# Optimization experiments

Hardware: AMD Instinct MI355X
Metric: run time of the kernel (lower is better)

Reference implementation:

```python
import jax, jax.numpy as jnp
import numpy as np

NUM_HEADS = 8
TEMPERATURE = 10000.0


def sine_embed(pos, dim):
    """Sine positional embedding of 2D offsets. pos [..., 2] -> [..., dim]."""
    half = dim // 2  # dims per coordinate
    dim_t = TEMPERATURE ** (2.0 * (jnp.arange(half) // 2).astype(jnp.float32) / half)
    s = pos[..., :, None] / dim_t  # [..., 2, half]
    emb = jnp.stack([jnp.sin(s[..., 0::2]), jnp.cos(s[..., 1::2])], axis=-1)
    emb = emb.reshape(s.shape[:-1] + (half,))  # interleaved sin/cos per coord
    return emb.reshape(pos.shape[:-1] + (dim,))


def setup_inputs() -> dict:
    key = jax.random.key(0)
    ks = jax.random.split(key, 16)
    N, H, W, C, K = 2, 40, 40, 256, 100
    h = NUM_HEADS
    sc = 1.0 / np.sqrt(C)
    return {
        "query_feature": jax.random.normal(ks[0], (N, H, W, C), jnp.float32),
        "query_position": jax.random.uniform(ks[1], (N, H, W, 2), jnp.float32),
        "key_feature": jax.random.normal(ks[2], (N, K, C), jnp.float32),
        "key_position": jax.random.uniform(ks[3], (N, K, 2), jnp.float32),
        # MultiheadAttention params (torch convention: weight [out, in])
        "in_proj_w": jax.random.normal(ks[4], (3 * C, C), jnp.float32) * sc,
        "in_proj_b": jnp.zeros((3 * C,), jnp.float32),
        "out_proj_w": jax.random.normal(ks[5], (C, C), jnp.float32) * sc,
        "out_proj_b": jnp.zeros((C,), jnp.float32),
        # PositionalEncodingSineLearned MLP: sine(C) -> C -> num_heads
        "pos_w1": jax.random.normal(ks[6], (C, C), jnp.float32) * sc,
        "pos_b1": jnp.zeros((C,), jnp.float32),
        "pos_w2": jax.random.normal(ks[7], (h, C), jnp.float32) * sc,
        "pos_b2": jnp.zeros((h,), jnp.float32),
        # cat_pos branch params
        "pos_trans_w": jax.random.normal(ks[8], (2, 2), jnp.float32),
        "embed_w": jax.random.normal(ks[9], (C, C + 2), jnp.float32) * 0.01,
        "embed_b": jnp.zeros((C,), jnp.float32),
    }


def reference(query_feature, query_position, key_feature, key_position,
              in_proj_w, in_proj_b, out_proj_w, out_proj_b,
              pos_w1, pos_b1, pos_w2, pos_b2,
              pos_trans_w, embed_w, embed_b):
    N, H, W, C = query_feature.shape
    h = NUM_HEADS
    d = C // h
    q = query_feature.reshape(N, -1, C)            # [N,Q,C]
    qp = query_position.reshape(N, -1, 2)          # [N,Q,2] (scale_terms = 1.0)
    Q = q.shape[1]
    K = key_feature.shape[1]

    # pairwise relative positions: [N,Q,K,2]
    rel_pos = key_position[:, None, :, :] - qp[:, :, None, :]

    # learned sine relative positional encoding -> per-head additive bias
    pe = sine_embed(rel_pos, C)                              # [N,Q,K,C]
    hid = jax.nn.relu(pe @ pos_w1.T + pos_b1)                # [N,Q,K,C]
    bias = (hid @ pos_w2.T + pos_b2).transpose(0, 3, 1, 2)   # [N,h,Q,K]

    # multihead attention with additive relative bias
    wq, wk, wv = jnp.split(in_proj_w, 3, axis=0)
    bq, bk, bv = jnp.split(in_proj_b, 3, axis=0)
    qh = ((q @ wq.T + bq).reshape(N, Q, h, d)) * (d ** -0.5)
    kh = (key_feature @ wk.T + bk).reshape(N, K, h, d)
    vh = (key_feature @ wv.T + bv).reshape(N, K, h, d)
    scores = jnp.einsum('nqhd,nkhd->nhqk', qh, kh) + bias
    attn = jax.nn.softmax(scores, axis=-1)                   # [N,h,Q,K]
    ctx = jnp.einsum('nhqk,nkhd->nqhd', attn, vh).reshape(N, Q, C)
    refined = ctx @ out_proj_w.T + out_proj_b                # [N,Q,C]

    # cat_pos: attention-weighted relative position aggregation
    attn_w = attn.mean(axis=1)                               # [N,Q,K]
    new_rel = jnp.einsum('nqk,nqkc->nqc', attn_w, jax.lax.stop_gradient(rel_pos))
    new_pos = new_rel @ pos_trans_w.T                        # [N,Q,2]

    feat = jax.nn.relu(q + refined)
    feat = jax.nn.relu(jnp.concatenate([feat, new_pos], axis=-1) @ embed_w.T + embed_b)
    return feat.reshape(N, H, W, C)
```

## Files before the change

### kernel.cpp

```cpp
#include <hip/hip_runtime.h>
#include <math.h>

typedef __bf16 bf16x8 __attribute__((ext_vector_type(8)));
typedef __bf16 bf16x4 __attribute__((ext_vector_type(4)));
typedef float  f32x4  __attribute__((ext_vector_type(4)));


#define WS_KH    0u
#define WS_VH    51200u
#define WS_EWP   102400u
#define WS_QHB   168960u
#define WS_BIASB 578560u
#define WS_KEB   2012160u
#define WS_W1B   2038560u
#define WS_W2PB  2071328u

__device__ __forceinline__ float rdlane(float v, int l) {
  return __uint_as_float(__builtin_amdgcn_readlane(__float_as_uint(v), l));
}

__global__ __launch_bounds__(256, 2) void prep_kernel(
    const float* __restrict__ qfeat, const float* __restrict__ kfeat,
    const float* __restrict__ kpos,
    const float* __restrict__ ipw, const float* __restrict__ ipb,
    const float* __restrict__ pos_w1, const float* __restrict__ pos_w2,
    const float* __restrict__ embed_w, float* __restrict__ ws)
{
  __shared__ float x[8 * 256];
  int bid = blockIdx.x, t = threadIdx.x;

  if (bid < 50) {
    int r = bid * 4 + (t >> 6);
    int u = t & 63;
    float p0 = kpos[r * 2 + 0], p1 = kpos[r * 2 + 1];
    __bf16* keb = (__bf16*)(ws + WS_KEB);
    bf16x4 o;
#pragma unroll
    for (int j = 0; j < 4; j++) {
      int col = u * 4 + j;
      int c = col >> 7, i = (col & 127) >> 1;
      float p = c ? p1 : p0;
      float inv = exp2f((float)i * (-13.287712379549449f / 64.0f));
      float v = p * inv;
      o[j] = (__bf16)((col & 1) ? __cosf(v) : __sinf(v));
    }
    *(bf16x4*)(keb + r * 264 + u * 4) = o;
  } else if (bid < 114) {
    int idx = (bid - 50) * 1024 + t * 4;
    float4 v = *(const float4*)(pos_w1 + idx);
    bf16x4 o; o[0] = (__bf16)v.x; o[1] = (__bf16)v.y; o[2] = (__bf16)v.z; o[3] = (__bf16)v.w;
    *(bf16x4*)((__bf16*)(ws + WS_W1B) + idx) = o;
  } else if (bid == 114) {
    __bf16* w2pb = (__bf16*)(ws + WS_W2PB);
    for (int i = 0; i < 16; i++) {
      int idx = t * 16 + i;
      w2pb[idx] = (idx < 2048) ? (__bf16)pos_w2[idx] : (__bf16)0.0f;
    }
  } else if (bid < 147) {
    int r0 = (bid - 115) * 8;
    for (int rr = 0; rr < 8; rr++) {
      int r = r0 + rr;
      for (int j = t; j < 260; j += 256)
        ws[WS_EWP + r * 260 + j] = (j < 258) ? embed_w[r * 258 + j] : 0.0f;
    }
  } else if (bid < 547) {
    int r0 = (bid - 147) * 8;
    for (int i = t; i < 2048; i += 256) x[i] = qfeat[(unsigned)r0 * 256u + i];
    __syncthreads();
    float acc[8]; float bq = ipb[t];
#pragma unroll
    for (int rr = 0; rr < 8; rr++) acc[rr] = bq;
    const float* wrow = ipw + (unsigned)t * 256u;
    for (int j = 0; j < 256; j += 4) {
      float4 w4 = *(const float4*)(wrow + j);
#pragma unroll
      for (int rr = 0; rr < 8; rr++) {
        float4 x4 = *(const float4*)(x + rr * 256 + j);
        acc[rr] = fmaf(x4.x, w4.x, fmaf(x4.y, w4.y, fmaf(x4.z, w4.z, fmaf(x4.w, w4.w, acc[rr]))));
      }
    }
    __bf16* qhb = (__bf16*)(ws + WS_QHB);
#pragma unroll
    for (int rr = 0; rr < 8; rr++)
      qhb[(unsigned)(r0 + rr) * 256u + t] = (__bf16)(acc[rr] * 0.17677669529663687f);
  } else {
    int b2 = bid - 547; int n = b2 >> 4, tile = b2 & 15;
    int r0l = tile * 7; int cnt = 100 - r0l; if (cnt > 7) cnt = 7; if (cnt <= 0) return;
    int r0 = n * 100 + r0l;
    for (int i = t; i < cnt * 256; i += 256) x[i] = kfeat[(unsigned)r0 * 256u + i];
    __syncthreads();
    float ak[7], av[7]; float bk = ipb[256 + t], bv = ipb[512 + t];
#pragma unroll
    for (int rr = 0; rr < 7; rr++) { ak[rr] = bk; av[rr] = bv; }
    const float* wkr = ipw + (unsigned)(256 + t) * 256u;
    const float* wvr = ipw + (unsigned)(512 + t) * 256u;
    for (int j = 0; j < 256; j += 4) {
      float4 wk4 = *(const float4*)(wkr + j);
      float4 wv4 = *(const float4*)(wvr + j);
#pragma unroll
      for (int rr = 0; rr < 7; rr++) {
        float4 x4 = *(const float4*)(x + rr * 256 + j);
        ak[rr] = fmaf(x4.x, wk4.x, fmaf(x4.y, wk4.y, fmaf(x4.z, wk4.z, fmaf(x4.w, wk4.w, ak[rr]))));
        av[rr] = fmaf(x4.x, wv4.x, fmaf(x4.y, wv4.y, fmaf(x4.z, wv4.z, fmaf(x4.w, wv4.w, av[rr]))));
      }
    }
    for (int rr = 0; rr < 7; rr++) {
      if (rr < cnt) {
        ws[WS_KH + (unsigned)(r0 + rr) * 256u + t] = ak[rr];
        ws[WS_VH + (unsigned)(r0 + rr) * 256u + t] = av[rr];
      }
    }
  }
}

__global__ __launch_bounds__(512) void bias_kernel(
    const float* __restrict__ qpos,
    const float* __restrict__ pos_b1, const float* __restrict__ pos_b2,
    float* __restrict__ ws)
{
  __shared__ __align__(16) char smem[63488];
  __bf16* qe_s   = (__bf16*)(smem + 28672);
  __bf16* region = (__bf16*)(smem + 30720);

  int bid = blockIdx.x;
  int n = bid / 400;
  int q0 = bid * 4;
  int t = threadIdx.x;
  int lane = t & 63, w = t >> 6;
  int l15 = lane & 15, quad = lane >> 4;

  const __bf16* keb = (const __bf16*)(ws + WS_KEB) + (unsigned)(n * 100) * 264u;
  const __bf16* w1b = (const __bf16*)(ws + WS_W1B);
  const __bf16* w2pb = (const __bf16*)(ws + WS_W2PB);
  __bf16* biasb = (__bf16*)(ws + WS_BIASB);

  {
    int idx = t * 2;
    int q = idx >> 8, u = idx & 255;
    int c = u >> 7, i = (u & 127) >> 1;
    float p = qpos[(q0 + q) * 2 + c];
    float inv = exp2f((float)i * (-13.287712379549449f / 64.0f));
    float v = p * inv;
    qe_s[idx]     = (__bf16)__sinf(v);
    qe_s[idx + 1] = (__bf16)__cosf(v);
  }

  bf16x8 wfrag[2][8];
#pragma unroll
  for (int ct = 0; ct < 2; ct++)
#pragma unroll
    for (int kc = 0; kc < 8; kc++)
      wfrag[ct][kc] = *(const bf16x8*)(w1b + (unsigned)(w * 32 + ct * 16 + l15) * 256u + kc * 32 + quad * 8);
  float b1v[2][4];
#pragma unroll
  for (int ct = 0; ct < 2; ct++)
#pragma unroll
    for (int r = 0; r < 4; r++) b1v[ct][r] = pos_b1[w * 32 + ct * 16 + quad * 4 + r];
  float b2v[4];
#pragma unroll
  for (int r = 0; r < 4; r++) b2v[r] = pos_b2[(quad * 4 + r) & 7];

  auto gen = [&](int q, int pair, int buf) {
    if (t < 448) {
      int key = t >> 2, sub = t & 3;
      int cb = pair * 64 + sub * 16;
      bf16x8 fr0, fr1;
      const __bf16* qp = qe_s + q * 256 + cb;
      bf16x8 q0f = *(const bf16x8*)qp;
      bf16x8 q1f = *(const bf16x8*)(qp + 8);
      if (key < 100) {
        const __bf16* kp = keb + (unsigned)key * 264u + cb;
        bf16x8 k0f = *(const bf16x8*)kp;
        bf16x8 k1f = *(const bf16x8*)(kp + 8);
#pragma unroll
        for (int jj = 0; jj < 4; jj++) {
          float sk = (float)k0f[2 * jj], ck = (float)k0f[2 * jj + 1];
          float sq = (float)q0f[2 * jj], cq = (float)q0f[2 * jj + 1];
          fr0[2 * jj]     = (__bf16)(sk * cq - ck * sq);
          fr0[2 * jj + 1] = (__bf16)(ck * cq + sk * sq);
          float sk1 = (float)k1f[2 * jj], ck1 = (float)k1f[2 * jj + 1];
          float sq1 = (float)q1f[2 * jj], cq1 = (float)q1f[2 * jj + 1];
          fr1[2 * jj]     = (__bf16)(sk1 * cq1 - ck1 * sq1);
          fr1[2 * jj + 1] = (__bf16)(ck1 * cq1 + sk1 * sq1);
        }
      } else {
#pragma unroll
        for (int jj = 0; jj < 8; jj++) { fr0[jj] = (__bf16)0.f; fr1[jj] = (__bf16)0.f; }
      }
      int mt = key >> 4, kl = key & 15;
      int kcl = sub >> 1;
      int qd0 = (sub & 1) * 2;
      bf16x8* base = (bf16x8*)smem + buf * 896 + kcl * 448 + mt * 64;
      base[qd0 * 16 + (kl ^ (qd0 * 2 + kcl))]             = fr0;
      base[(qd0 + 1) * 16 + (kl ^ (qd0 * 2 + 2 + kcl))]   = fr1;
    }
  };

  f32x4 zero4; zero4[0] = 0.f; zero4[1] = 0.f; zero4[2] = 0.f; zero4[3] = 0.f;

  __syncthreads();
  gen(0, 0, 0);
  __syncthreads();

  for (int q = 0; q < 4; q++) {
    f32x4 acc[2][7];
#pragma unroll
    for (int ct = 0; ct < 2; ct++)
#pragma unroll
      for (int mt = 0; mt < 7; mt++) acc[ct][mt] = zero4;

    for (int p = 0; p < 4; p++) {
      if (p < 3) gen(q, p + 1, (p + 1) & 1);
      else if (q < 3) gen(q + 1, 0, 0);
      const bf16x8* pb = (const bf16x8*)smem + (p & 1) * 896;
#pragma unroll
      for (int kh = 0; kh < 2; kh++) {
        int kc = p * 2 + kh;
        bf16x8 pf[7];
#pragma unroll
        for (int mt = 0; mt < 7; mt++)
          pf[mt] = pb[kh * 448 + mt * 64 + quad * 16 + (l15 ^ (quad * 2 + kh))];
#pragma unroll
        for (int mt = 0; mt < 7; mt++) {
          acc[0][mt] = __builtin_amdgcn_mfma_f32_16x16x32_bf16(wfrag[0][kc], pf[mt], acc[0][mt], 0, 0, 0);
          acc[1][mt] = __builtin_amdgcn_mfma_f32_16x16x32_bf16(wfrag[1][kc], pf[mt], acc[1][mt], 0, 0, 0);
        }
      }
      __syncthreads();
    }

#pragma unroll
    for (int ct = 0; ct < 2; ct++)
#pragma unroll
      for (int mt = 0; mt < 7; mt++)
#pragma unroll
        for (int r = 0; r < 4; r++)
          acc[ct][mt][r] = fmaxf(acc[ct][mt][r] + b1v[ct][r], 0.0f);

    auto wreg = [&](int mt, int slot) {
#pragma unroll
      for (int ct = 0; ct < 2; ct++) {
        int qt = ct * 2 + (quad >> 1);
        int j0 = (quad & 1) * 4;
        bf16x4 o;
#pragma unroll
        for (int r = 0; r < 4; r++) o[r] = (__bf16)acc[ct][mt][r];
        *(bf16x4*)(region + slot * 4096 + ((w * 64 + qt * 16 + l15) << 3) + j0) = o;
      }
    };
    auto g2 = [&](int mt, int slot) {
      f32x4 acc2 = zero4;
      const bf16x8* rg = (const bf16x8*)(region + slot * 4096);
#pragma unroll
      for (int s = 0; s < 8; s++) {
        bf16x8 w2f = *(const bf16x8*)(w2pb + (unsigned)l15 * 256u + s * 32 + quad * 8);
        bf16x8 hf = rg[s * 64 + lane];
        acc2 = __builtin_amdgcn_mfma_f32_16x16x32_bf16(w2f, hf, acc2, 0, 0, 0);
      }
      if (quad < 2) {
        bf16x4 o;
#pragma unroll
        for (int r = 0; r < 4; r++) o[r] = (__bf16)(acc2[r] + b2v[r]);
        *(bf16x4*)(biasb + ((unsigned)(q0 + q) * 112u + mt * 16 + l15) * 8u + quad * 4) = o;
      }
    };

    wreg(0, 0); wreg(1, 1); wreg(2, 2); wreg(3, 3);
    __syncthreads();
    if (w < 4) g2(w, w);
    __syncthreads();
    wreg(4, 0); wreg(5, 1); wreg(6, 2);
    __syncthreads();
    if (w < 3) g2(4 + w, w);
  }
}

__global__ __launch_bounds__(256, 4) void attn_kernel(
    const float* __restrict__ qfeat, const float* __restrict__ qpos,
    const float* __restrict__ kpos,
    const float* __restrict__ out_w, const float* __restrict__ out_b,
    const float* __restrict__ embed_b, const float* __restrict__ ptw,
    const float* __restrict__ ws, float* __restrict__ out)
{
  __shared__ float qh_s[4 * 8 * 36];
  __shared__ float attn_s[4 * 8 * 116];
  __shared__ float ctx_s[4 * 264];
  __shared__ float cat_s[4 * 264];
  __shared__ float aw_s[4 * 104];

  int bid = blockIdx.x;
  int qg0 = bid * 4;
  int n = bid / 400;
  int t = threadIdx.x;

  const __bf16* qhb = (const __bf16*)(ws + WS_QHB);
  const __bf16* biasb = (const __bf16*)(ws + WS_BIASB);
  const float* kh = ws + WS_KH;
  const float* vh = ws + WS_VH;
  const float* ewp = ws + WS_EWP;

  for (int i = t; i < 1024; i += 256) {
    int q = i >> 8, c = i & 255;
    qh_s[(q * 8 + (c >> 5)) * 36 + (c & 31)] = (float)qhb[(unsigned)(qg0 + q) * 256u + c];
  }
  __syncthreads();

  for (int i = 0; i < 4; i++) {
    int p = t + i * 256;
    if (p < 800) {
      int k = p >> 3, h = p & 7;
      const float4* kf = (const float4*)(kh + (unsigned)(n * 100 + k) * 256u + h * 32);
      float4 kv[8];
#pragma unroll
      for (int dd = 0; dd < 8; dd++) kv[dd] = kf[dd];
#pragma unroll
      for (int q = 0; q < 4; q++) {
        const float4* qf = (const float4*)(qh_s + (q * 8 + h) * 36);
        float s = (float)biasb[((unsigned)(qg0 + q) * 112u + k) * 8u + h];
#pragma unroll
        for (int dd = 0; dd < 8; dd++) {
          float4 qv = qf[dd];
          s += kv[dd].x * qv.x + kv[dd].y * qv.y + kv[dd].z * qv.z + kv[dd].w * qv.w;
        }
        attn_s[(q * 8 + h) * 116 + k] = s;
      }
    }
  }
  __syncthreads();

  {
    int q = t >> 6, h = (t >> 3) & 7, j = t & 7;
    float* row = attn_s + (q * 8 + h) * 116;
    float mx = -1e30f;
    for (int k = j; k < 100; k += 8) mx = fmaxf(mx, row[k]);
    mx = fmaxf(mx, __shfl_xor(mx, 1, 8));
    mx = fmaxf(mx, __shfl_xor(mx, 2, 8));
    mx = fmaxf(mx, __shfl_xor(mx, 4, 8));
    float sum = 0.f;
    for (int k = j; k < 100; k += 8) { float e = __expf(row[k] - mx); row[k] = e; sum += e; }
    sum += __shfl_xor(sum, 1, 8);
    sum += __shfl_xor(sum, 2, 8);
    sum += __shfl_xor(sum, 4, 8);
    float inv = 1.0f / sum;
    for (int k = j; k < 100; k += 8) row[k] *= inv;
  }
  __syncthreads();

  for (int p = t; p < 416; p += 256) {
    int q = p / 104, k = p % 104;
    if (k < 100) {
      float s = 0.f;
#pragma unroll
      for (int h = 0; h < 8; h++) s += attn_s[(q * 8 + h) * 116 + k];
      aw_s[q * 104 + k] = s * 0.125f;
    }
  }
  {
    int c = t, h = c >> 5;
    float a0 = 0.f, a1 = 0.f, a2 = 0.f, a3 = 0.f;
    const float* vp = vh + (unsigned)(n * 100) * 256u + c;
    const float* r0 = attn_s + (0 * 8 + h) * 116;
    const float* r1 = attn_s + (1 * 8 + h) * 116;
    const float* r2 = attn_s + (2 * 8 + h) * 116;
    const float* r3 = attn_s + (3 * 8 + h) * 116;
#pragma unroll 4
    for (int k = 0; k < 100; k++) {
      float vv = vp[(unsigned)k * 256u];
      a0 = fmaf(r0[k], vv, a0);
      a1 = fmaf(r1[k], vv, a1);
      a2 = fmaf(r2[k], vv, a2);
      a3 = fmaf(r3[k], vv, a3);
    }
    ctx_s[0 * 264 + c] = a0; ctx_s[1 * 264 + c] = a1;
    ctx_s[2 * 264 + c] = a2; ctx_s[3 * 264 + c] = a3;
  }
  __syncthreads();

  if (t < 8) {
    int q = t >> 1, cd = t & 1;
    float qp = qpos[(qg0 + q) * 2 + cd];
    float s = 0.f;
    for (int k = 0; k < 100; k++)
      s = fmaf(aw_s[q * 104 + k], kpos[(n * 100 + k) * 2 + cd] - qp, s);
    float so = __shfl_xor(s, 1, 2);
    if (cd == 0) cat_s[q * 264 + 256] = ptw[0] * s + ptw[1] * so;
    else         cat_s[q * 264 + 257] = ptw[2] * so + ptw[3] * s;
  }

  {
    int c = t, lane = t & 63;
    float ob = out_b[c];
    float acc0 = ob, acc1 = ob, acc2 = ob, acc3 = ob;
    const float* wr = out_w + (unsigned)c * 256u;
    for (int ch = 0; ch < 4; ch++) {
      float v0 = ctx_s[0 * 264 + ch * 64 + lane];
      float v1 = ctx_s[1 * 264 + ch * 64 + lane];
      float v2 = ctx_s[2 * 264 + ch * 64 + lane];
      float v3 = ctx_s[3 * 264 + ch * 64 + lane];
      const float* wp = wr + ch * 64;
#pragma unroll 4
      for (int j4 = 0; j4 < 16; j4++) {
        float4 w4 = *(const float4*)(wp + j4 * 4);
        int jb = j4 * 4;
        acc0 = fmaf(rdlane(v0, jb + 0), w4.x, acc0);
        acc1 = fmaf(rdlane(v1, jb + 0), w4.x, acc1);
        acc2 = fmaf(rdlane(v2, jb + 0), w4.x, acc2);
        acc3 = fmaf(rdlane(v3, jb + 0), w4.x, acc3);
        acc0 = fmaf(rdlane(v0, jb + 1), w4.y, acc0);
        acc1 = fmaf(rdlane(v1, jb + 1), w4.y, acc1);
        acc2 = fmaf(rdlane(v2, jb + 1), w4.y, acc2);
        acc3 = fmaf(rdlane(v3, jb + 1), w4.y, acc3);
        acc0 = fmaf(rdlane(v0, jb + 2), w4.z, acc0);
        acc1 = fmaf(rdlane(v1, jb + 2), w4.z, acc1);
        acc2 = fmaf(rdlane(v2, jb + 2), w4.z, acc2);
        acc3 = fmaf(rdlane(v3, jb + 2), w4.z, acc3);
        acc0 = fmaf(rdlane(v0, jb + 3), w4.w, acc0);
        acc1 = fmaf(rdlane(v1, jb + 3), w4.w, acc1);
        acc2 = fmaf(rdlane(v2, jb + 3), w4.w, acc2);
        acc3 = fmaf(rdlane(v3, jb + 3), w4.w, acc3);
      }
    }
    cat_s[0 * 264 + c] = fmaxf(qfeat[(unsigned)(qg0 + 0) * 256u + c] + acc0, 0.f);
    cat_s[1 * 264 + c] = fmaxf(qfeat[(unsigned)(qg0 + 1) * 256u + c] + acc1, 0.f);
    cat_s[2 * 264 + c] = fmaxf(qfeat[(unsigned)(qg0 + 2) * 256u + c] + acc2, 0.f);
    cat_s[3 * 264 + c] = fmaxf(qfeat[(unsigned)(qg0 + 3) * 256u + c] + acc3, 0.f);
  }
  __syncthreads();

  {
    int c = t, lane = t & 63;
    float eb = embed_b[c];
    float acc0 = eb, acc1 = eb, acc2 = eb, acc3 = eb;
    const float* er = ewp + (unsigned)c * 260u;
    for (int ch = 0; ch < 4; ch++) {
      float v0 = cat_s[0 * 264 + ch * 64 + lane];
      float v1 = cat_s[1 * 264 + ch * 64 + lane];
      float v2 = cat_s[2 * 264 + ch * 64 + lane];
      float v3 = cat_s[3 * 264 + ch * 64 + lane];
      const float* wp = er + ch * 64;
#pragma unroll 4
      for (int j4 = 0; j4 < 16; j4++) {
        float4 w4 = *(const float4*)(wp + j4 * 4);
        int jb = j4 * 4;
        acc0 = fmaf(rdlane(v0, jb + 0), w4.x, acc0);
        acc1 = fmaf(rdlane(v1, jb + 0), w4.x, acc1);
        acc2 = fmaf(rdlane(v2, jb + 0), w4.x, acc2);
        acc3 = fmaf(rdlane(v3, jb + 0), w4.x, acc3);
        acc0 = fmaf(rdlane(v0, jb + 1), w4.y, acc0);
        acc1 = fmaf(rdlane(v1, jb + 1), w4.y, acc1);
        acc2 = fmaf(rdlane(v2, jb + 1), w4.y, acc2);
        acc3 = fmaf(rdlane(v3, jb + 1), w4.y, acc3);
        acc0 = fmaf(rdlane(v0, jb + 2), w4.z, acc0);
        acc1 = fmaf(rdlane(v1, jb + 2), w4.z, acc1);
        acc2 = fmaf(rdlane(v2, jb + 2), w4.z, acc2);
        acc3 = fmaf(rdlane(v3, jb + 2), w4.z, acc3);
        acc0 = fmaf(rdlane(v0, jb + 3), w4.w, acc0);
        acc1 = fmaf(rdlane(v1, jb + 3), w4.w, acc1);
        acc2 = fmaf(rdlane(v2, jb + 3), w4.w, acc2);
        acc3 = fmaf(rdlane(v3, jb + 3), w4.w, acc3);
      }
    }
    float4 wt = *(const float4*)(er + 256);
    acc0 += cat_s[0 * 264 + 256] * wt.x + cat_s[0 * 264 + 257] * wt.y;
    acc1 += cat_s[1 * 264 + 256] * wt.x + cat_s[1 * 264 + 257] * wt.y;
    acc2 += cat_s[2 * 264 + 256] * wt.x + cat_s[2 * 264 + 257] * wt.y;
    acc3 += cat_s[3 * 264 + 256] * wt.x + cat_s[3 * 264 + 257] * wt.y;
    out[(unsigned)(qg0 + 0) * 256u + c] = fmaxf(acc0, 0.f);
    out[(unsigned)(qg0 + 1) * 256u + c] = fmaxf(acc1, 0.f);
    out[(unsigned)(qg0 + 2) * 256u + c] = fmaxf(acc2, 0.f);
    out[(unsigned)(qg0 + 3) * 256u + c] = fmaxf(acc3, 0.f);
  }
}

extern "C" void kernel_launch(void* const* d_in, const int* in_sizes, int n_in,
                              void* d_out, int out_size, void* d_ws, size_t ws_size,
                              hipStream_t stream)
{
  const float* query_feature  = (const float*)d_in[0];
  const float* query_position = (const float*)d_in[1];
  const float* key_feature    = (const float*)d_in[2];
  const float* key_position   = (const float*)d_in[3];
  const float* in_proj_w      = (const float*)d_in[4];
  const float* in_proj_b      = (const float*)d_in[5];
  const float* out_proj_w     = (const float*)d_in[6];
  const float* out_proj_b     = (const float*)d_in[7];
  const float* pos_w1         = (const float*)d_in[8];
  const float* pos_b1         = (const float*)d_in[9];
  const float* pos_w2         = (const float*)d_in[10];
  const float* pos_b2         = (const float*)d_in[11];
  const float* pos_trans_w    = (const float*)d_in[12];
  const float* embed_w        = (const float*)d_in[13];
  const float* embed_b        = (const float*)d_in[14];
  float* ws  = (float*)d_ws;
  float* out = (float*)d_out;

  hipLaunchKernelGGL(prep_kernel, dim3(579), dim3(256), 0, stream,
                     query_feature, key_feature, key_position,
                     in_proj_w, in_proj_b, pos_w1, pos_w2, embed_w, ws);
  hipLaunchKernelGGL(bias_kernel, dim3(800), dim3(512), 0, stream,
                     query_position, pos_b1, pos_b2, ws);
  hipLaunchKernelGGL(attn_kernel, dim3(800), dim3(256), 0, stream,
                     query_feature, query_position, key_position,
                     out_proj_w, out_proj_b, embed_b, pos_trans_w,
                     ws, out);
}
```

Baseline: 295.1 us.

## Transpose projection weights for coalesced access, split prep, pipeline bias generation

Adds a prep pass that transposes embed, out_proj and in_proj weights (in_proj into bf16), so that GEMV loops in prep2 and attn_kernel read one coalesced column per thread instead of strided per-thread rows. The bias generator is split into a load phase issued before the MFMA loop and a compute/store phase after it, so LDS loads overlap with matrix work. The bias buffer is compacted from 112 to 100 keys per query to cut its writes and reads. This costs one extra kernel launch, and the bf16 in_proj weights reduce projection precision.

```diff
diff --git a/kernel.cpp b/kernel.cpp
--- a/kernel.cpp
+++ b/kernel.cpp
@@ -5,28 +5,28 @@
 typedef __bf16 bf16x4 __attribute__((ext_vector_type(4)));
 typedef float  f32x4  __attribute__((ext_vector_type(4)));
 
-
 #define WS_KH    0u
 #define WS_VH    51200u
-#define WS_EWP   102400u
-#define WS_QHB   168960u
-#define WS_BIASB 578560u
-#define WS_KEB   2012160u
-#define WS_W1B   2038560u
-#define WS_W2PB  2071328u
+#define WS_EWT   102400u
+#define WS_OWT   168448u
+#define WS_QHB   233984u
+#define WS_BIASB 643584u
+#define WS_KEB   1923584u
+#define WS_W1B   1949984u
+#define WS_W2PB  1982752u
+#define WS_IPWT  1984800u
 
 __device__ __forceinline__ float rdlane(float v, int l) {
   return __uint_as_float(__builtin_amdgcn_readlane(__float_as_uint(v), l));
 }
 
-__global__ __launch_bounds__(256, 2) void prep_kernel(
-    const float* __restrict__ qfeat, const float* __restrict__ kfeat,
+__global__ __launch_bounds__(256) void prep1_kernel(
     const float* __restrict__ kpos,
-    const float* __restrict__ ipw, const float* __restrict__ ipb,
     const float* __restrict__ pos_w1, const float* __restrict__ pos_w2,
-    const float* __restrict__ embed_w, float* __restrict__ ws)
+    const float* __restrict__ embed_w, const float* __restrict__ out_w,
+    const float* __restrict__ ipw, float* __restrict__ ws)
 {
-  __shared__ float x[8 * 256];
+  __shared__ float tile[64 * 65];
   int bid = blockIdx.x, t = threadIdx.x;
 
   if (bid < 50) {
@@ -56,27 +56,79 @@
       int idx = t * 16 + i;
       w2pb[idx] = (idx < 2048) ? (__bf16)pos_w2[idx] : (__bf16)0.0f;
     }
-  } else if (bid < 147) {
-    int r0 = (bid - 115) * 8;
-    for (int rr = 0; rr < 8; rr++) {
-      int r = r0 + rr;
-      for (int j = t; j < 260; j += 256)
-        ws[WS_EWP + r * 260 + j] = (j < 258) ? embed_w[r * 258 + j] : 0.0f;
-    }
-  } else if (bid < 547) {
-    int r0 = (bid - 147) * 8;
+  } else if (bid < 135) {
+    int idx = bid - 115;
+    int j0 = (idx / 4) * 64, c0 = (idx % 4) * 64;
+    int jj = t & 63, rq = t >> 6;
+    for (int rr = 0; rr < 16; rr++) {
+      int c = rr * 4 + rq;
+      float v = (j0 + jj < 258) ? embed_w[(c0 + c) * 258 + j0 + jj] : 0.0f;
+      tile[c * 65 + jj] = v;
+    }
+    __syncthreads();
+    int cc = t & 63, jq = t >> 6;
+    for (int pp = 0; pp < 16; pp++) {
+      int j = pp * 4 + jq;
+      if (j0 + j < 258)
+        ws[WS_EWT + (unsigned)(j0 + j) * 256u + c0 + cc] = tile[cc * 65 + j];
+    }
+  } else if (bid < 151) {
+    int idx = bid - 135;
+    int j0 = (idx >> 2) * 64, c0 = (idx & 3) * 64;
+    int jj = t & 63, rq = t >> 6;
+    for (int rr = 0; rr < 16; rr++) {
+      int c = rr * 4 + rq;
+      tile[c * 65 + jj] = out_w[(c0 + c) * 256 + j0 + jj];
+    }
+    __syncthreads();
+    int cc = t & 63, jq = t >> 6;
+    for (int pp = 0; pp < 16; pp++) {
+      int j = pp * 4 + jq;
+      ws[WS_OWT + (unsigned)(j0 + j) * 256u + c0 + cc] = tile[cc * 65 + j];
+    }
+  } else {
+    int idx = bid - 151;
+    int j0 = (idx & 3) * 64, o0 = (idx >> 2) * 64;
+    int jj = t & 63, rq = t >> 6;
+    for (int rr = 0; rr < 16; rr++) {
+      int o = rr * 4 + rq;
+      tile[o * 65 + jj] = ipw[(unsigned)(o0 + o) * 256u + j0 + jj];
+    }
+    __syncthreads();
+    __bf16* ipwt = (__bf16*)(ws + WS_IPWT);
+    int oo = t & 63, jq = t >> 6;
+    for (int pp = 0; pp < 16; pp++) {
+      int j = pp * 4 + jq;
+      ipwt[(unsigned)(j0 + j) * 768u + o0 + oo] = (__bf16)tile[oo * 65 + j];
+    }
+  }
+}
+
+__global__ __launch_bounds__(256, 2) void prep2_kernel(
+    const float* __restrict__ qfeat, const float* __restrict__ kfeat,
+    const float* __restrict__ ipb, float* __restrict__ ws)
+{
+  __shared__ float x[8 * 256];
+  int bid = blockIdx.x, t = threadIdx.x;
+  const __bf16* ipwt = (const __bf16*)(ws + WS_IPWT);
+
+  if (bid < 400) {
+    int r0 = bid * 8;
     for (int i = t; i < 2048; i += 256) x[i] = qfeat[(unsigned)r0 * 256u + i];
     __syncthreads();
     float acc[8]; float bq = ipb[t];
 #pragma unroll
     for (int rr = 0; rr < 8; rr++) acc[rr] = bq;
-    const float* wrow = ipw + (unsigned)t * 256u;
+#pragma unroll 4
     for (int j = 0; j < 256; j += 4) {
-      float4 w4 = *(const float4*)(wrow + j);
+      float w0 = (float)ipwt[(unsigned)(j + 0) * 768u + t];
+      float w1 = (float)ipwt[(unsigned)(j + 1) * 768u + t];
+      float w2 = (float)ipwt[(unsigned)(j + 2) * 768u + t];
+      float w3 = (float)ipwt[(unsigned)(j + 3) * 768u + t];
 #pragma unroll
       for (int rr = 0; rr < 8; rr++) {
         float4 x4 = *(const float4*)(x + rr * 256 + j);
-        acc[rr] = fmaf(x4.x, w4.x, fmaf(x4.y, w4.y, fmaf(x4.z, w4.z, fmaf(x4.w, w4.w, acc[rr]))));
+        acc[rr] = fmaf(x4.x, w0, fmaf(x4.y, w1, fmaf(x4.z, w2, fmaf(x4.w, w3, acc[rr]))));
       }
     }
     __bf16* qhb = (__bf16*)(ws + WS_QHB);
@@ -84,24 +136,29 @@
     for (int rr = 0; rr < 8; rr++)
       qhb[(unsigned)(r0 + rr) * 256u + t] = (__bf16)(acc[rr] * 0.17677669529663687f);
   } else {
-    int b2 = bid - 547; int n = b2 >> 4, tile = b2 & 15;
-    int r0l = tile * 7; int cnt = 100 - r0l; if (cnt > 7) cnt = 7; if (cnt <= 0) return;
+    int b2 = bid - 400; int n = b2 >> 4, tileI = b2 & 15;
+    int r0l = tileI * 7; int cnt = 100 - r0l; if (cnt > 7) cnt = 7; if (cnt <= 0) return;
     int r0 = n * 100 + r0l;
     for (int i = t; i < cnt * 256; i += 256) x[i] = kfeat[(unsigned)r0 * 256u + i];
     __syncthreads();
     float ak[7], av[7]; float bk = ipb[256 + t], bv = ipb[512 + t];
 #pragma unroll
     for (int rr = 0; rr < 7; rr++) { ak[rr] = bk; av[rr] = bv; }
-    const float* wkr = ipw + (unsigned)(256 + t) * 256u;
-    const float* wvr = ipw + (unsigned)(512 + t) * 256u;
+#pragma unroll 2
     for (int j = 0; j < 256; j += 4) {
-      float4 wk4 = *(const float4*)(wkr + j);
-      float4 wv4 = *(const float4*)(wvr + j);
+      float wk0 = (float)ipwt[(unsigned)(j + 0) * 768u + 256 + t];
+      float wk1 = (float)ipwt[(unsigned)(j + 1) * 768u + 256 + t];
+      float wk2 = (float)ipwt[(unsigned)(j + 2) * 768u + 256 + t];
+      float wk3 = (float)ipwt[(unsigned)(j + 3) * 768u + 256 + t];
+      float wv0 = (float)ipwt[(unsigned)(j + 0) * 768u + 512 + t];
+      float wv1 = (float)ipwt[(unsigned)(j + 1) * 768u + 512 + t];
+      float wv2 = (float)ipwt[(unsigned)(j + 2) * 768u + 512 + t];
+      float wv3 = (float)ipwt[(unsigned)(j + 3) * 768u + 512 + t];
 #pragma unroll
       for (int rr = 0; rr < 7; rr++) {
         float4 x4 = *(const float4*)(x + rr * 256 + j);
-        ak[rr] = fmaf(x4.x, wk4.x, fmaf(x4.y, wk4.y, fmaf(x4.z, wk4.z, fmaf(x4.w, wk4.w, ak[rr]))));
-        av[rr] = fmaf(x4.x, wv4.x, fmaf(x4.y, wv4.y, fmaf(x4.z, wv4.z, fmaf(x4.w, wv4.w, av[rr]))));
+        ak[rr] = fmaf(x4.x, wk0, fmaf(x4.y, wk1, fmaf(x4.z, wk2, fmaf(x4.w, wk3, ak[rr]))));
+        av[rr] = fmaf(x4.x, wv0, fmaf(x4.y, wv1, fmaf(x4.z, wv2, fmaf(x4.w, wv3, av[rr]))));
       }
     }
     for (int rr = 0; rr < 7; rr++) {
@@ -160,26 +217,37 @@
 #pragma unroll
   for (int r = 0; r < 4; r++) b2v[r] = pos_b2[(quad * 4 + r) & 7];
 
-  auto gen = [&](int q, int pair, int buf) {
-    if (t < 448) {
-      int key = t >> 2, sub = t & 3;
-      int cb = pair * 64 + sub * 16;
+  bool gact = (t < 448);
+  int gkey = t >> 2, gsub = t & 3;
+  int gmt = gkey >> 4, gkl = gkey & 15;
+  int gkcl = gsub >> 1, gqd0 = (gsub & 1) * 2;
+  bf16x8 gk0, gk1, gq0, gq1;
+
+  auto gen_load = [&](int q, int pair) {
+    if (gact) {
+      int cb = pair * 64 + gsub * 16;
+      const __bf16* qp = qe_s + q * 256 + cb;
+      gq0 = *(const bf16x8*)qp;
+      gq1 = *(const bf16x8*)(qp + 8);
+      if (gkey < 100) {
+        const __bf16* kp = keb + (unsigned)gkey * 264u + cb;
+        gk0 = *(const bf16x8*)kp;
+        gk1 = *(const bf16x8*)(kp + 8);
+      }
+    }
+  };
+  auto gen_store = [&](int buf) {
+    if (gact) {
       bf16x8 fr0, fr1;
-      const __bf16* qp = qe_s + q * 256 + cb;
-      bf16x8 q0f = *(const bf16x8*)qp;
-      bf16x8 q1f = *(const bf16x8*)(qp + 8);
-      if (key < 100) {
-        const __bf16* kp = keb + (unsigned)key * 264u + cb;
-        bf16x8 k0f = *(const bf16x8*)kp;
-        bf16x8 k1f = *(const bf16x8*)(kp + 8);
+      if (gkey < 100) {
 #pragma unroll
         for (int jj = 0; jj < 4; jj++) {
-          float sk = (float)k0f[2 * jj], ck = (float)k0f[2 * jj + 1];
-          float sq = (float)q0f[2 * jj], cq = (float)q0f[2 * jj + 1];
+          float sk = (float)gk0[2 * jj], ck = (float)gk0[2 * jj + 1];
+          float sq = (float)gq0[2 * jj], cq = (float)gq0[2 * jj + 1];
           fr0[2 * jj]     = (__bf16)(sk * cq - ck * sq);
           fr0[2 * jj + 1] = (__bf16)(ck * cq + sk * sq);
-          float sk1 = (float)k1f[2 * jj], ck1 = (float)k1f[2 * jj + 1];
-          float sq1 = (float)q1f[2 * jj], cq1 = (float)q1f[2 * jj + 1];
+          float sk1 = (float)gk1[2 * jj], ck1 = (float)gk1[2 * jj + 1];
+          float sq1 = (float)gq1[2 * jj], cq1 = (float)gq1[2 * jj + 1];
           fr1[2 * jj]     = (__bf16)(sk1 * cq1 - ck1 * sq1);
           fr1[2 * jj + 1] = (__bf16)(ck1 * cq1 + sk1 * sq1);
         }
@@ -187,19 +255,17 @@
 #pragma unroll
         for (int jj = 0; jj < 8; jj++) { fr0[jj] = (__bf16)0.f; fr1[jj] = (__bf16)0.f; }
       }
-      int mt = key >> 4, kl = key & 15;
-      int kcl = sub >> 1;
-      int qd0 = (sub & 1) * 2;
-      bf16x8* base = (bf16x8*)smem + buf * 896 + kcl * 448 + mt * 64;
-      base[qd0 * 16 + (kl ^ (qd0 * 2 + kcl))]             = fr0;
-      base[(qd0 + 1) * 16 + (kl ^ (qd0 * 2 + 2 + kcl))]   = fr1;
+      bf16x8* base = (bf16x8*)smem + buf * 896 + gkcl * 448 + gmt * 64;
+      base[gqd0 * 16 + (gkl ^ (gqd0 * 2 + gkcl))]           = fr0;
+      base[(gqd0 + 1) * 16 + (gkl ^ (gqd0 * 2 + 2 + gkcl))] = fr1;
     }
   };
 
   f32x4 zero4; zero4[0] = 0.f; zero4[1] = 0.f; zero4[2] = 0.f; zero4[3] = 0.f;
 
   __syncthreads();
-  gen(0, 0, 0);
+  gen_load(0, 0);
+  gen_store(0);
   __syncthreads();
 
   for (int q = 0; q < 4; q++) {
@@ -210,8 +276,14 @@
       for (int mt = 0; mt < 7; mt++) acc[ct][mt] = zero4;
 
     for (int p = 0; p < 4; p++) {
-      if (p < 3) gen(q, p + 1, (p + 1) & 1);
-      else if (q < 3) gen(q + 1, 0, 0);
+      int nq = q, npair = p + 1, nbuf = (p + 1) & 1;
+      bool have_next = true;
+      if (p == 3) {
+        if (q < 3) { nq = q + 1; npair = 0; nbuf = 0; }
+        else have_next = false;
+      }
+      if (have_next) gen_load(nq, npair);
+
       const bf16x8* pb = (const bf16x8*)smem + (p & 1) * 896;
 #pragma unroll
       for (int kh = 0; kh < 2; kh++) {
@@ -226,6 +298,7 @@
           acc[1][mt] = __builtin_amdgcn_mfma_f32_16x16x32_bf16(wfrag[1][kc], pf[mt], acc[1][mt], 0, 0, 0);
         }
       }
+      if (have_next) gen_store(nbuf);
       __syncthreads();
     }
 
@@ -258,10 +331,13 @@
         acc2 = __builtin_amdgcn_mfma_f32_16x16x32_bf16(w2f, hf, acc2, 0, 0, 0);
       }
       if (quad < 2) {
-        bf16x4 o;
-#pragma unroll
-        for (int r = 0; r < 4; r++) o[r] = (__bf16)(acc2[r] + b2v[r]);
-        *(bf16x4*)(biasb + ((unsigned)(q0 + q) * 112u + mt * 16 + l15) * 8u + quad * 4) = o;
+        int key = mt * 16 + l15;
+        if (key < 100) {
+          bf16x4 o;
+#pragma unroll
+          for (int r = 0; r < 4; r++) o[r] = (__bf16)(acc2[r] + b2v[r]);
+          *(bf16x4*)(biasb + ((unsigned)(q0 + q) * 100u + key) * 8u + quad * 4) = o;
+        }
       }
     };
 
@@ -278,8 +354,8 @@
 __global__ __launch_bounds__(256, 4) void attn_kernel(
     const float* __restrict__ qfeat, const float* __restrict__ qpos,
     const float* __restrict__ kpos,
-    const float* __restrict__ out_w, const float* __restrict__ out_b,
-    const float* __restrict__ embed_b, const float* __restrict__ ptw,
+    const float* __restrict__ out_b, const float* __restrict__ embed_b,
+    const float* __restrict__ ptw,
     const float* __restrict__ ws, float* __restrict__ out)
 {
   __shared__ float qh_s[4 * 8 * 36];
@@ -297,7 +373,8 @@
   const __bf16* biasb = (const __bf16*)(ws + WS_BIASB);
   const float* kh = ws + WS_KH;
   const float* vh = ws + WS_VH;
-  const float* ewp = ws + WS_EWP;
+  const float* owt = ws + WS_OWT;
+  const float* ewt = ws + WS_EWT;
 
   for (int i = t; i < 1024; i += 256) {
     int q = i >> 8, c = i & 255;
@@ -316,7 +393,7 @@
 #pragma unroll
       for (int q = 0; q < 4; q++) {
         const float4* qf = (const float4*)(qh_s + (q * 8 + h) * 36);
-        float s = (float)biasb[((unsigned)(qg0 + q) * 112u + k) * 8u + h];
+        float s = (float)biasb[((unsigned)(qg0 + q) * 100u + k) * 8u + h];
 #pragma unroll
         for (int dd = 0; dd < 8; dd++) {
           float4 qv = qf[dd];
@@ -391,33 +468,19 @@
     int c = t, lane = t & 63;
     float ob = out_b[c];
     float acc0 = ob, acc1 = ob, acc2 = ob, acc3 = ob;
-    const float* wr = out_w + (unsigned)c * 256u;
     for (int ch = 0; ch < 4; ch++) {
       float v0 = ctx_s[0 * 264 + ch * 64 + lane];
       float v1 = ctx_s[1 * 264 + ch * 64 + lane];
       float v2 = ctx_s[2 * 264 + ch * 64 + lane];
       float v3 = ctx_s[3 * 264 + ch * 64 + lane];
-      const float* wp = wr + ch * 64;
-#pragma unroll 4
-      for (int j4 = 0; j4 < 16; j4++) {
-        float4 w4 = *(const float4*)(wp + j4 * 4);
-        int jb = j4 * 4;
-        acc0 = fmaf(rdlane(v0, jb + 0), w4.x, acc0);
-        acc1 = fmaf(rdlane(v1, jb + 0), w4.x, acc1);
-        acc2 = fmaf(rdlane(v2, jb + 0), w4.x, acc2);
-        acc3 = fmaf(rdlane(v3, jb + 0), w4.x, acc3);
-        acc0 = fmaf(rdlane(v0, jb + 1), w4.y, acc0);
-        acc1 = fmaf(rdlane(v1, jb + 1), w4.y, acc1);
-        acc2 = fmaf(rdlane(v2, jb + 1), w4.y, acc2);
-        acc3 = fmaf(rdlane(v3, jb + 1), w4.y, acc3);
-        acc0 = fmaf(rdlane(v0, jb + 2), w4.z, acc0);
-        acc1 = fmaf(rdlane(v1, jb + 2), w4.z, acc1);
-        acc2 = fmaf(rdlane(v2, jb + 2), w4.z, acc2);
-        acc3 = fmaf(rdlane(v3, jb + 2), w4.z, acc3);
-        acc0 = fmaf(rdlane(v0, jb + 3), w4.w, acc0);
-        acc1 = fmaf(rdlane(v1, jb + 3), w4.w, acc1);
-        acc2 = fmaf(rdlane(v2, jb + 3), w4.w, acc2);
-        acc3 = fmaf(rdlane(v3, jb + 3), w4.w, acc3);
+      const float* wp = owt + (unsigned)(ch * 64) * 256u + c;
+#pragma unroll 8
+      for (int j2 = 0; j2 < 64; j2++) {
+        float wv = wp[(unsigned)j2 * 256u];
+        acc0 = fmaf(rdlane(v0, j2), wv, acc0);
+        acc1 = fmaf(rdlane(v1, j2), wv, acc1);
+        acc2 = fmaf(rdlane(v2, j2), wv, acc2);
+        acc3 = fmaf(rdlane(v3, j2), wv, acc3);
       }
     }
     cat_s[0 * 264 + c] = fmaxf(qfeat[(unsigned)(qg0 + 0) * 256u + c] + acc0, 0.f);
@@ -431,40 +494,27 @@
     int c = t, lane = t & 63;
     float eb = embed_b[c];
     float acc0 = eb, acc1 = eb, acc2 = eb, acc3 = eb;
-    const float* er = ewp + (unsigned)c * 260u;
     for (int ch = 0; ch < 4; ch++) {
       float v0 = cat_s[0 * 264 + ch * 64 + lane];
       float v1 = cat_s[1 * 264 + ch * 64 + lane];
       float v2 = cat_s[2 * 264 + ch * 64 + lane];
       float v3 = cat_s[3 * 264 + ch * 64 + lane];
-      const float* wp = er + ch * 64;
-#pragma unroll 4
-      for (int j4 = 0; j4 < 16; j4++) {
-        float4 w4 = *(const float4*)(wp + j4 * 4);
-        int jb = j4 * 4;
-        acc0 = fmaf(rdlane(v0, jb + 0), w4.x, acc0);
-        acc1 = fmaf(rdlane(v1, jb + 0), w4.x, acc1);
-        acc2 = fmaf(rdlane(v2, jb + 0), w4.x, acc2);
-        acc3 = fmaf(rdlane(v3, jb + 0), w4.x, acc3);
-        acc0 = fmaf(rdlane(v0, jb + 1), w4.y, acc0);
-        acc1 = fmaf(rdlane(v1, jb + 1), w4.y, acc1);
-        acc2 = fmaf(rdlane(v2, jb + 1), w4.y, acc2);
-        acc3 = fmaf(rdlane(v3, jb + 1), w4.y, acc3);
-        acc0 = fmaf(rdlane(v0, jb + 2), w4.z, acc0);
-        acc1 = fmaf(rdlane(v1, jb + 2), w4.z, acc1);
-        acc2 = fmaf(rdlane(v2, jb + 2), w4.z, acc2);
-        acc3 = fmaf(rdlane(v3, jb + 2), w4.z, acc3);
-        acc0 = fmaf(rdlane(v0, jb + 3), w4.w, acc0);
-        acc1 = fmaf(rdlane(v1, jb + 3), w4.w, acc1);
-        acc2 = fmaf(rdlane(v2, jb + 3), w4.w, acc2);
-        acc3 = fmaf(rdlane(v3, jb + 3), w4.w, acc3);
-      }
-    }
-    float4 wt = *(const float4*)(er + 256);
-    acc0 += cat_s[0 * 264 + 256] * wt.x + cat_s[0 * 264 + 257] * wt.y;
-    acc1 += cat_s[1 * 264 + 256] * wt.x + cat_s[1 * 264 + 257] * wt.y;
-    acc2 += cat_s[2 * 264 + 256] * wt.x + cat_s[2 * 264 + 257] * wt.y;
-    acc3 += cat_s[3 * 264 + 256] * wt.x + cat_s[3 * 264 + 257] * wt.y;
+      const float* wp = ewt + (unsigned)(ch * 64) * 256u + c;
+#pragma unroll 8
+      for (int j2 = 0; j2 < 64; j2++) {
+        float wv = wp[(unsigned)j2 * 256u];
+        acc0 = fmaf(rdlane(v0, j2), wv, acc0);
+        acc1 = fmaf(rdlane(v1, j2), wv, acc1);
+        acc2 = fmaf(rdlane(v2, j2), wv, acc2);
+        acc3 = fmaf(rdlane(v3, j2), wv, acc3);
+      }
+    }
+    float w256 = ewt[256u * 256u + c];
+    float w257 = ewt[257u * 256u + c];
+    acc0 += cat_s[0 * 264 + 256] * w256 + cat_s[0 * 264 + 257] * w257;
+    acc1 += cat_s[1 * 264 + 256] * w256 + cat_s[1 * 264 + 257] * w257;
+    acc2 += cat_s[2 * 264 + 256] * w256 + cat_s[2 * 264 + 257] * w257;
+    acc3 += cat_s[3 * 264 + 256] * w256 + cat_s[3 * 264 + 257] * w257;
     out[(unsigned)(qg0 + 0) * 256u + c] = fmaxf(acc0, 0.f);
     out[(unsigned)(qg0 + 1) * 256u + c] = fmaxf(acc1, 0.f);
     out[(unsigned)(qg0 + 2) * 256u + c] = fmaxf(acc2, 0.f);
@@ -494,13 +544,15 @@
   float* ws  = (float*)d_ws;
   float* out = (float*)d_out;
 
-  hipLaunchKernelGGL(prep_kernel, dim3(579), dim3(256), 0, stream,
-                     query_feature, key_feature, key_position,
-                     in_proj_w, in_proj_b, pos_w1, pos_w2, embed_w, ws);
+  hipLaunchKernelGGL(prep1_kernel, dim3(199), dim3(256), 0, stream,
+                     key_position, pos_w1, pos_w2, embed_w, out_proj_w,
+                     in_proj_w, ws);
+  hipLaunchKernelGGL(prep2_kernel, dim3(432), dim3(256), 0, stream,
+                     query_feature, key_feature, in_proj_b, ws);
   hipLaunchKernelGGL(bias_kernel, dim3(800), dim3(512), 0, stream,
                      query_position, pos_b1, pos_b2, ws);
   hipLaunchKernelGGL(attn_kernel, dim3(800), dim3(256), 0, stream,
                      query_feature, query_position, key_position,
-                     out_proj_w, out_proj_b, embed_b, pos_trans_w,
+                     out_proj_b, embed_b, pos_trans_w,
                      ws, out);
 }
```

After: 299.7 us. About the same (+1.5%).
